# Performance work log

Measured on AMD Instinct MI355X. Metric: run time of the kernel, lower is better.

The kernel has to match this reference:

```python
import jax, jax.numpy as jnp
import numpy as np

B, D, T, H, E = 4, 1024, 2048, 16, 64  # batch, dim, seq_len, n_heads, hidden_dim (H*E == D)


def setup_inputs() -> dict:
    key = jax.random.key(0)
    ks = jax.random.split(key, 6)
    x = jax.random.normal(ks[0], (B, D, T), dtype=jnp.float32)            # (b, e, t) layout
    Wp = jax.random.normal(ks[1], (H, E, D), dtype=jnp.float32) / np.sqrt(D)  # per-head proj weights
    bp = jax.random.normal(ks[2], (H, E), dtype=jnp.float32) * 0.01
    tw = jax.random.normal(ks[3], (H, T), dtype=jnp.float32) / np.sqrt(T)  # per-head Toeplitz kernel, tw[h,0]=diagonal
    Wo = jax.random.normal(ks[4], (D, D), dtype=jnp.float32) / np.sqrt(D)
    bo = jax.random.normal(ks[5], (D,), dtype=jnp.float32) * 0.01
    return {"x": x, "Wp": Wp, "bp": bp, "tw": tw, "Wo": Wo, "bo": bo}


def reference(x, Wp, bp, tw, Wo, bo):
    # x: (b, dim, t) -> (b, t, dim)
    xt = jnp.transpose(x, (0, 2, 1))
    # per-head projections: (b, h, e, t)
    proj = jnp.einsum('btd,hed->bhet', xt, Wp) + bp[None, :, :, None]
    # build per-head causal lower-triangular Toeplitz matrices: Tm[h, t, s] = tw[h, t-s] if s <= t else 0
    idx = jnp.arange(T)[:, None] - jnp.arange(T)[None, :]  # (t, s)
    Tm = jnp.where(idx >= 0, tw[:, jnp.clip(idx, 0)], 0.0)  # (h, t, s)
    # causal Toeplitz mixing along time per head
    mixed = jnp.einsum('hts,bhes->bhet', Tm, proj)          # (b, h, e, t)
    # concat heads on feature dim: (b, t, h*e) == (b, t, dim)
    cat = jnp.transpose(mixed, (0, 3, 1, 2)).reshape(B, T, H * E)
    out = cat @ Wo.T + bo                                   # out_proj: Linear(dim, dim)
    return jnp.transpose(out, (0, 2, 1))                    # back to (b, e, t)
```

## Files before the change

kernel.cpp:

```cpp
#include <hip/hip_runtime.h>
#include <cstdint>

#define NB 4
#define ND 1024
#define NT 2048
#define NH 16
#define NE 64
#define GLEN 2240
#define CAP 2312

typedef __bf16 bf16x8 __attribute__((ext_vector_type(8)));
typedef float f32x4 __attribute__((ext_vector_type(4)));
typedef unsigned short us8 __attribute__((ext_vector_type(8)));

__device__ __forceinline__ unsigned short f2bf(float f) {
  unsigned u = __builtin_bit_cast(unsigned, f);
  return (unsigned short)((u + 0x7fffu + ((u >> 16) & 1u)) >> 16);
}

__device__ __forceinline__ void gload16(const void* g, void* l) {
  __builtin_amdgcn_global_load_lds(
      (const __attribute__((address_space(1))) void*)(uintptr_t)g,
      (__attribute__((address_space(3))) void*)(uintptr_t)l, 16, 0, 0);
}

__global__ void prep_kernel(const float* __restrict__ Wp, const float* __restrict__ Wo,
                            const float* __restrict__ tw,
                            unsigned short* __restrict__ WpB, unsigned short* __restrict__ WoB,
                            unsigned short* __restrict__ Gr8) {
  int idx = blockIdx.x * 256 + threadIdx.x;
  int stride = gridDim.x * 256;
  for (int i = idx; i < ND * ND; i += stride) WpB[i] = f2bf(Wp[i]);
  for (int i = idx; i < ND * ND; i += stride) WoB[i] = f2bf(Wo[i]);
  for (int i = idx; i < NH * 8 * GLEN; i += stride) {
    int h = i / (8 * GLEN);
    int rem = i - h * 8 * GLEN;
    int r = rem / GLEN;
    int c = rem - r * GLEN;
    int src = c + r;
    Gr8[i] = (src <= NT - 1) ? f2bf(tw[h * NT + (NT - 1) - src]) : (unsigned short)0;
  }
}

__global__ __launch_bounds__(256) void transpose_cast(const float* __restrict__ x,
                                                      unsigned short* __restrict__ xT) {
  __shared__ float tile[32][33];
  int tx = threadIdx.x & 31, ty = threadIdx.x >> 5;
  int t0 = blockIdx.x * 32, d0 = blockIdx.y * 32, b = blockIdx.z;
  const float* xb = x + (long)b * ND * NT;
#pragma unroll
  for (int k = 0; k < 4; ++k)
    tile[ty + 8 * k][tx] = xb[(long)(d0 + ty + 8 * k) * NT + t0 + tx];
  __syncthreads();
  unsigned short* xTb = xT + (long)b * NT * ND;
#pragma unroll
  for (int k = 0; k < 4; ++k)
    xTb[(long)(t0 + ty + 8 * k) * ND + d0 + tx] = f2bf(tile[tx][ty + 8 * k]);
}

template <bool OUT_BF16>
__global__ __launch_bounds__(256, 2) void gemm_bt(const unsigned short* __restrict__ A,
                                                  const unsigned short* __restrict__ Bt,
                                                  const float* __restrict__ bias,
                                                  void* __restrict__ Cb, long strideB,
                                                  long strideC) {
  const int N = 2048, K = 1024;
  __shared__ __align__(16) unsigned short As[128 * 32];
  __shared__ __align__(16) unsigned short Bs[128 * 32];
  const int tid = threadIdx.x;
  const int lane = tid & 63;
  const int wid = tid >> 6;
  const int wm = (wid & 1) * 64, wn = (wid >> 1) * 64;
  const int m0 = blockIdx.y * 128, n0 = blockIdx.x * 128;
  const unsigned short* Bb = Bt + (long)blockIdx.z * strideB;
  const int mlo = lane & 15, q = lane >> 4;

  f32x4 acc[4][4] = {};
  for (int k0 = 0; k0 < K; k0 += 32) {
#pragma unroll
    for (int p = 0; p < 2; ++p) {
      int idx = p * 256 + tid;
      int row = idx >> 2, kc = (idx & 3) * 8;
      gload16(A + (long)(m0 + row) * K + k0 + kc, &As[idx * 8]);
      gload16(Bb + (long)(n0 + row) * K + k0 + kc, &Bs[idx * 8]);
    }
    __syncthreads();
    bf16x8 av[4], bv[4];
#pragma unroll
    for (int i = 0; i < 4; ++i) {
      av[i] = __builtin_bit_cast(bf16x8, *(const us8*)&As[(wm + i * 16 + mlo) * 32 + q * 8]);
      bv[i] = __builtin_bit_cast(bf16x8, *(const us8*)&Bs[(wn + i * 16 + mlo) * 32 + q * 8]);
    }
#pragma unroll
    for (int i = 0; i < 4; ++i)
#pragma unroll
      for (int j = 0; j < 4; ++j)
        acc[i][j] = __builtin_amdgcn_mfma_f32_16x16x32_bf16(av[i], bv[j], acc[i][j], 0, 0, 0);
    __syncthreads();
  }
#pragma unroll
  for (int i = 0; i < 4; ++i)
#pragma unroll
    for (int j = 0; j < 4; ++j)
#pragma unroll
      for (int r = 0; r < 4; ++r) {
        int gr = m0 + wm + i * 16 + q * 4 + r;
        int gc = n0 + wn + j * 16 + mlo;
        float v = acc[i][j][r] + bias[gr];
        if (OUT_BF16)
          ((unsigned short*)Cb)[(long)blockIdx.z * strideC + (long)gr * N + gc] = f2bf(v);
        else
          ((float*)Cb)[(long)blockIdx.z * strideC + (long)gr * N + gc] = v;
      }
}

__global__ __launch_bounds__(256, 3) void toeplitz(const unsigned short* __restrict__ proj,
                                                   const unsigned short* __restrict__ Gr8,
                                                   unsigned short* __restrict__ mixedT) {
  __shared__ __align__(16) unsigned short Ls[8 * CAP];
  __shared__ __align__(16) unsigned short Bs[128 * 32];
  const int tid = threadIdx.x, lane = tid & 63, w = tid >> 6;
  const int t0 = ((int)gridDim.x - 1 - (int)blockIdx.x) * 128;
  const int h = blockIdx.y, zb = blockIdx.z;
  const int mlo = lane & 15, q = lane >> 4;
  const int wt = (w & 1) * 64, wn = (w >> 1) * 64;

  const int delta = (NT - 128) - t0;
  const int MUSE = t0 + 256;
#pragma unroll 1
  for (int r = 0; r < 8; ++r) {
    int rr = (r + delta) & 7;
    int off8 = r + delta - rr;
    const unsigned short* src = Gr8 + (long)(h * 8 + rr) * GLEN + off8;
    unsigned short* dst = &Ls[r * CAP];
    for (int mc = tid; mc * 8 < MUSE; mc += 256) gload16(src + mc * 8, &dst[mc * 8]);
  }

  const int rA = (7 - mlo) & 7;
  const unsigned short* lA = &Ls[rA * CAP + (127 - wt - mlo - rA) + q * 8];

  f32x4 acc[4][4] = {};
  const int kend = t0 + 128;
  for (int s0 = 0; s0 < kend; s0 += 32) {
#pragma unroll
    for (int p = 0; p < 2; ++p) {
      int idx = p * 256 + tid;
      int n = idx >> 2, kc = (idx & 3) * 8;
      int bb = n >> 6, e = n & 63;
      gload16(proj + ((long)(zb * 2 + bb) * ND + h * 64 + e) * NT + s0 + kc, &Bs[idx * 8]);
    }
    __syncthreads();
    bf16x8 av[4], bv[4];
#pragma unroll
    for (int i = 0; i < 4; ++i)
      av[i] = __builtin_bit_cast(bf16x8, *(const us8*)(lA + s0 - i * 16));
#pragma unroll
    for (int j = 0; j < 4; ++j)
      bv[j] = __builtin_bit_cast(bf16x8, *(const us8*)&Bs[(wn + j * 16 + mlo) * 32 + q * 8]);
#pragma unroll
    for (int i = 0; i < 4; ++i)
#pragma unroll
      for (int j = 0; j < 4; ++j)
        acc[i][j] = __builtin_amdgcn_mfma_f32_16x16x32_bf16(av[i], bv[j], acc[i][j], 0, 0, 0);
    __syncthreads();
  }
#pragma unroll
  for (int i = 0; i < 4; ++i)
#pragma unroll
    for (int j = 0; j < 4; ++j)
#pragma unroll
      for (int rr = 0; rr < 4; ++rr) {
        int t = t0 + wt + i * 16 + q * 4 + rr;
        int n = wn + j * 16 + mlo;
        int bb = n >> 6, e = n & 63;
        mixedT[((long)(zb * 2 + bb) * NT + t) * ND + h * 64 + e] = f2bf(acc[i][j][rr]);
      }
}

extern "C" void kernel_launch(void* const* d_in, const int* in_sizes, int n_in, void* d_out,
                              int out_size, void* d_ws, size_t ws_size, hipStream_t stream) {
  const float* x = (const float*)d_in[0];
  const float* Wp = (const float*)d_in[1];
  const float* bp = (const float*)d_in[2];
  const float* tw = (const float*)d_in[3];
  const float* Wo = (const float*)d_in[4];
  const float* bo = (const float*)d_in[5];
  float* out = (float*)d_out;

  char* ws = (char*)d_ws;
  unsigned short* xT = (unsigned short*)(ws);
  unsigned short* proj = (unsigned short*)(ws + (16ull << 20));
  unsigned short* WpB = (unsigned short*)(ws + (32ull << 20));
  unsigned short* WoB = (unsigned short*)(ws + (34ull << 20));
  unsigned short* Gr8 = (unsigned short*)(ws + (36ull << 20));

  prep_kernel<<<dim3(2048), 256, 0, stream>>>(Wp, Wo, tw, WpB, WoB, Gr8);
  transpose_cast<<<dim3(NT / 32, ND / 32, NB), 256, 0, stream>>>(x, xT);
  gemm_bt<true><<<dim3(16, 8, NB), 256, 0, stream>>>(WpB, xT, bp, proj, (long)NT * ND,
                                                     (long)ND * NT);
  toeplitz<<<dim3(NT / 128, NH, NB / 2), 256, 0, stream>>>(proj, Gr8, xT);
  gemm_bt<false><<<dim3(16, 8, NB), 256, 0, stream>>>(WoB, xT, bo, out, (long)NT * ND,
                                                      (long)ND * NT);
}
```

Before: 189.4 us.

## Pair causal Toeplitz tiles per block, double-buffer B, and reuse A fragments

The Toeplitz kernel now handles one batch per block, and each block processes two time tiles: a long one (15-j) and a short one (j). This balances the triangular work evenly across blocks, and the grid changes to 8x16x4. The B tile is shrunk to 64 rows and double-buffered, so global-to-LDS loads overlap the MFMAs. A fragments are reused across k-steps through a sliding window (ap0/ap1) because of the Toeplitz structure, which halves LDS reads for A. Occupancy drops from 3 to 2 blocks per CU, and each block runs more serial work.

```diff
diff --git a/kernel.cpp b/kernel.cpp
--- a/kernel.cpp
+++ b/kernel.cpp
@@ -114,67 +114,93 @@
       }
 }
 
-__global__ __launch_bounds__(256, 3) void toeplitz(const unsigned short* __restrict__ proj,
+__global__ __launch_bounds__(256, 2) void toeplitz(const unsigned short* __restrict__ proj,
                                                    const unsigned short* __restrict__ Gr8,
                                                    unsigned short* __restrict__ mixedT) {
   __shared__ __align__(16) unsigned short Ls[8 * CAP];
-  __shared__ __align__(16) unsigned short Bs[128 * 32];
+  __shared__ __align__(16) unsigned short Bs[2][64 * 32];
   const int tid = threadIdx.x, lane = tid & 63, w = tid >> 6;
-  const int t0 = ((int)gridDim.x - 1 - (int)blockIdx.x) * 128;
-  const int h = blockIdx.y, zb = blockIdx.z;
+  const int j = blockIdx.x, h = blockIdx.y, bz = blockIdx.z;
   const int mlo = lane & 15, q = lane >> 4;
-  const int wt = (w & 1) * 64, wn = (w >> 1) * 64;
-
-  const int delta = (NT - 128) - t0;
-  const int MUSE = t0 + 256;
+  const int wt = (w >> 1) * 64, we = (w & 1) * 32;
+  const int t0L = (15 - j) * 128, t0S = j * 128;
+
+  const int delta = (NT - 128) - t0L;
+  const int MUSE = t0L + 256;
 #pragma unroll 1
   for (int r = 0; r < 8; ++r) {
     int rr = (r + delta) & 7;
     int off8 = r + delta - rr;
     const unsigned short* src = Gr8 + (long)(h * 8 + rr) * GLEN + off8;
     unsigned short* dst = &Ls[r * CAP];
-    for (int mc = tid; mc * 8 < MUSE; mc += 256) gload16(src + mc * 8, &dst[mc * 8]);
+    for (int mc = tid; mc * 8 < MUSE; mc += 256) gload16(src + mc * 8, dst + mc * 8);
   }
 
   const int rA = (7 - mlo) & 7;
-  const unsigned short* lA = &Ls[rA * CAP + (127 - wt - mlo - rA) + q * 8];
-
-  f32x4 acc[4][4] = {};
-  const int kend = t0 + 128;
-  for (int s0 = 0; s0 < kend; s0 += 32) {
-#pragma unroll
-    for (int p = 0; p < 2; ++p) {
-      int idx = p * 256 + tid;
-      int n = idx >> 2, kc = (idx & 3) * 8;
-      int bb = n >> 6, e = n & 63;
-      gload16(proj + ((long)(zb * 2 + bb) * ND + h * 64 + e) * NT + s0 + kc, &Bs[idx * 8]);
+  const int eRow = tid >> 2, kCol = (tid & 3) * 8;
+  const unsigned short* bsrc = proj + ((long)bz * ND + h * 64 + eRow) * NT + kCol;
+
+#pragma unroll 1
+  for (int p = 0; p < 2; ++p) {
+    const int t0p = p ? t0S : t0L;
+    const int kend = t0p + 128;
+    const unsigned short* lA =
+        &Ls[rA * CAP + (127 - wt - mlo - rA) + q * 8 + (t0L - t0p)];
+    gload16(bsrc, &Bs[0][tid * 8]);
+    __syncthreads();
+    bf16x8 ap0 = __builtin_bit_cast(bf16x8, *(const us8*)(lA - 32));
+    bf16x8 ap1 = __builtin_bit_cast(bf16x8, *(const us8*)(lA - 48));
+    f32x4 acc[4][2] = {};
+#pragma unroll 1
+    for (int s0 = 0; s0 < kend; s0 += 64) {
+      gload16(bsrc + s0 + 32, &Bs[1][tid * 8]);
+      {
+        bf16x8 a0 = __builtin_bit_cast(bf16x8, *(const us8*)(lA + s0));
+        bf16x8 a1 = __builtin_bit_cast(bf16x8, *(const us8*)(lA + s0 - 16));
+        bf16x8 b0 = __builtin_bit_cast(bf16x8, *(const us8*)&Bs[0][(we + mlo) * 32 + q * 8]);
+        bf16x8 b1 = __builtin_bit_cast(bf16x8, *(const us8*)&Bs[0][(we + 16 + mlo) * 32 + q * 8]);
+        acc[0][0] = __builtin_amdgcn_mfma_f32_16x16x32_bf16(a0, b0, acc[0][0], 0, 0, 0);
+        acc[0][1] = __builtin_amdgcn_mfma_f32_16x16x32_bf16(a0, b1, acc[0][1], 0, 0, 0);
+        acc[1][0] = __builtin_amdgcn_mfma_f32_16x16x32_bf16(a1, b0, acc[1][0], 0, 0, 0);
+        acc[1][1] = __builtin_amdgcn_mfma_f32_16x16x32_bf16(a1, b1, acc[1][1], 0, 0, 0);
+        acc[2][0] = __builtin_amdgcn_mfma_f32_16x16x32_bf16(ap0, b0, acc[2][0], 0, 0, 0);
+        acc[2][1] = __builtin_amdgcn_mfma_f32_16x16x32_bf16(ap0, b1, acc[2][1], 0, 0, 0);
+        acc[3][0] = __builtin_amdgcn_mfma_f32_16x16x32_bf16(ap1, b0, acc[3][0], 0, 0, 0);
+        acc[3][1] = __builtin_amdgcn_mfma_f32_16x16x32_bf16(ap1, b1, acc[3][1], 0, 0, 0);
+        ap0 = a0;
+        ap1 = a1;
+      }
+      __syncthreads();
+      if (s0 + 64 < kend) gload16(bsrc + s0 + 64, &Bs[0][tid * 8]);
+      {
+        bf16x8 a0 = __builtin_bit_cast(bf16x8, *(const us8*)(lA + s0 + 32));
+        bf16x8 a1 = __builtin_bit_cast(bf16x8, *(const us8*)(lA + s0 + 16));
+        bf16x8 b0 = __builtin_bit_cast(bf16x8, *(const us8*)&Bs[1][(we + mlo) * 32 + q * 8]);
+        bf16x8 b1 = __builtin_bit_cast(bf16x8, *(const us8*)&Bs[1][(we + 16 + mlo) * 32 + q * 8]);
+        acc[0][0] = __builtin_amdgcn_mfma_f32_16x16x32_bf16(a0, b0, acc[0][0], 0, 0, 0);
+        acc[0][1] = __builtin_amdgcn_mfma_f32_16x16x32_bf16(a0, b1, acc[0][1], 0, 0, 0);
+        acc[1][0] = __builtin_amdgcn_mfma_f32_16x16x32_bf16(a1, b0, acc[1][0], 0, 0, 0);
+        acc[1][1] = __builtin_amdgcn_mfma_f32_16x16x32_bf16(a1, b1, acc[1][1], 0, 0, 0);
+        acc[2][0] = __builtin_amdgcn_mfma_f32_16x16x32_bf16(ap0, b0, acc[2][0], 0, 0, 0);
+        acc[2][1] = __builtin_amdgcn_mfma_f32_16x16x32_bf16(ap0, b1, acc[2][1], 0, 0, 0);
+        acc[3][0] = __builtin_amdgcn_mfma_f32_16x16x32_bf16(ap1, b0, acc[3][0], 0, 0, 0);
+        acc[3][1] = __builtin_amdgcn_mfma_f32_16x16x32_bf16(ap1, b1, acc[3][1], 0, 0, 0);
+        ap0 = a0;
+        ap1 = a1;
+      }
+      __syncthreads();
     }
-    __syncthreads();
-    bf16x8 av[4], bv[4];
 #pragma unroll
     for (int i = 0; i < 4; ++i)
-      av[i] = __builtin_bit_cast(bf16x8, *(const us8*)(lA + s0 - i * 16));
-#pragma unroll
-    for (int j = 0; j < 4; ++j)
-      bv[j] = __builtin_bit_cast(bf16x8, *(const us8*)&Bs[(wn + j * 16 + mlo) * 32 + q * 8]);
-#pragma unroll
-    for (int i = 0; i < 4; ++i)
-#pragma unroll
-      for (int j = 0; j < 4; ++j)
-        acc[i][j] = __builtin_amdgcn_mfma_f32_16x16x32_bf16(av[i], bv[j], acc[i][j], 0, 0, 0);
-    __syncthreads();
-  }
-#pragma unroll
-  for (int i = 0; i < 4; ++i)
-#pragma unroll
-    for (int j = 0; j < 4; ++j)
-#pragma unroll
-      for (int rr = 0; rr < 4; ++rr) {
-        int t = t0 + wt + i * 16 + q * 4 + rr;
-        int n = wn + j * 16 + mlo;
-        int bb = n >> 6, e = n & 63;
-        mixedT[((long)(zb * 2 + bb) * NT + t) * ND + h * 64 + e] = f2bf(acc[i][j][rr]);
-      }
+#pragma unroll
+      for (int jj = 0; jj < 2; ++jj)
+#pragma unroll
+        for (int rr = 0; rr < 4; ++rr) {
+          int t = t0p + wt + i * 16 + q * 4 + rr;
+          int e = we + jj * 16 + mlo;
+          mixedT[((long)bz * NT + t) * ND + h * 64 + e] = f2bf(acc[i][jj][rr]);
+        }
+  }
 }
 
 extern "C" void kernel_launch(void* const* d_in, const int* in_sizes, int n_in, void* d_out,
@@ -198,7 +224,7 @@
   transpose_cast<<<dim3(NT / 32, ND / 32, NB), 256, 0, stream>>>(x, xT);
   gemm_bt<true><<<dim3(16, 8, NB), 256, 0, stream>>>(WpB, xT, bp, proj, (long)NT * ND,
                                                      (long)ND * NT);
-  toeplitz<<<dim3(NT / 128, NH, NB / 2), 256, 0, stream>>>(proj, Gr8, xT);
+  toeplitz<<<dim3(8, NH, NB), 256, 0, stream>>>(proj, Gr8, xT);
   gemm_bt<false><<<dim3(16, 8, NB), 256, 0, stream>>>(WoB, xT, bo, out, (long)NT * ND,
                                                       (long)ND * NT);
 }
```

After: 176.4 us. -6.8%, faster.
